# Optimization experiments

Hardware: AMD Instinct MI355X
Metric: run time of the kernel (lower is better)

Reference implementation:

```python
import jax, jax.numpy as jnp
import numpy as np

B, C, H, W = 8, 512, 32, 32
HEADS, GROUPS = 8, 32
EPS = 1e-5


def setup_inputs() -> dict:
    key = jax.random.key(0)
    ks = jax.random.split(key, 6)
    s = 0.02
    return {
        "x": jax.random.normal(ks[0], (B, C, H, W), jnp.float32),
        "gn_scale": jnp.ones((C,), jnp.float32),
        "gn_bias": jnp.zeros((C,), jnp.float32),
        "wq": jax.random.normal(ks[1], (C, C), jnp.float32) * s,
        "bq": jnp.zeros((C,), jnp.float32),
        "wk": jax.random.normal(ks[2], (C, C), jnp.float32) * s,
        "bk": jnp.zeros((C,), jnp.float32),
        "wv": jax.random.normal(ks[3], (C, C), jnp.float32) * s,
        "bv": jnp.zeros((C,), jnp.float32),
        "wo": jax.random.normal(ks[4], (C, C), jnp.float32) * s,
        "bo": jnp.zeros((C,), jnp.float32),
    }


def reference(x, gn_scale, gn_bias, wq, bq, wk, bk, wv, bv, wo, bo):
    b, c, h, w = x.shape
    n = h * w
    cdh = c // HEADS
    xf = x.reshape(b, c, n)

    # GroupNorm over (channels_per_group, spatial)
    g = xf.reshape(b, GROUPS, (c // GROUPS) * n)
    mu = g.mean(-1, keepdims=True)
    var = g.var(-1, keepdims=True)
    hn = ((g - mu) * jax.lax.rsqrt(var + EPS)).reshape(b, c, n)
    hn = hn * gn_scale[:, None] + gn_bias[:, None]

    # 1x1 conv projections == channel-mixing GEMMs
    q = jnp.einsum('oc,bcn->bon', wq, hn) + bq[:, None]
    k = jnp.einsum('oc,bcn->bon', wk, hn) + bk[:, None]
    v = jnp.einsum('oc,bcn->bon', wv, hn) + bv[:, None]

    qh = q.reshape(b, HEADS, cdh, n)
    kh = k.reshape(b, HEADS, cdh, n)
    vh = v.reshape(b, HEADS, cdh, n)

    scale = 1.0 / jnp.sqrt(jnp.float32(cdh))
    scores = jnp.einsum('bhdq,bhdk->bhqk', qh, kh) * scale  # [B,H,N,N]
    attn = jax.nn.softmax(scores, axis=-1)  # dropout p=0.0 (eval) -> identity

    oh = jnp.einsum('bhqk,bhdk->bhdq', attn, vh).reshape(b, c, n)
    out = jnp.einsum('oc,bcn->bon', wo, oh) + bo[:, None]
    return (xf + out).reshape(b, c, h, w)
```

## Files before the change

### kernel.cpp

```cpp
#include <hip/hip_runtime.h>

#define BB 8
#define CC 512
#define NSP 1024
#define HEADS 8
#define DH 64
#define NGROUPS 32
#define CPG 16
#define GN_EPS 1e-5f
#define MQKV 1536

typedef __attribute__((ext_vector_type(8))) short bf16x8;
typedef __attribute__((ext_vector_type(4))) short short4v;
typedef __attribute__((ext_vector_type(4))) float f32x4;

typedef __attribute__((address_space(3))) unsigned int lds_u32;
typedef const __attribute__((address_space(1))) unsigned int glb_u32;

__device__ __forceinline__ short f2bf(float f) {
    union { float f; unsigned u; } v; v.f = f;
    unsigned r = v.u + 0x7fffu + ((v.u >> 16) & 1u);
    return (short)(r >> 16);
}
__device__ __forceinline__ short f2bf_trunc(float f) {
    union { float f; unsigned u; } v; v.f = f;
    return (short)(v.u >> 16);
}

__device__ __forceinline__ float wave_reduce_sum(float v) {
    #pragma unroll
    for (int off = 32; off > 0; off >>= 1) v += __shfl_down(v, off, 64);
    return v;
}

#define QSCALE 0.18033688011112042f

__global__ __launch_bounds__(256) void convert_w_kernel(
        const float* __restrict__ wq, const float* __restrict__ wk,
        const float* __restrict__ wv, const float* __restrict__ wo,
        const float* __restrict__ bq, const float* __restrict__ bk,
        const float* __restrict__ bv,
        short* __restrict__ wqkv, short* __restrict__ wob,
        float* __restrict__ bqkv) {
    const int gid = blockIdx.x * 256 + threadIdx.x;
    if (gid < MQKV * CC) {
        const int r = gid >> 9;
        const int cc = gid & 511;
        const float* src = (r < 512) ? wq : ((r < 1024) ? wk : wv);
        float v = src[(size_t)(r & 511) * CC + cc];
        if (r < 512) v *= QSCALE;
        wqkv[gid] = f2bf(v);
    } else {
        const int g2 = gid - MQKV * CC;
        wob[g2] = f2bf(wo[g2]);
    }
    if (gid < MQKV) {
        float bvv = (gid < 512) ? bq[gid] * QSCALE
                  : ((gid < 1024) ? bk[gid - 512] : bv[gid - 1024]);
        bqkv[gid] = bvv;
    }
}

__global__ __launch_bounds__(256) void groupnorm_t_kernel(
        const float* __restrict__ x, const float* __restrict__ gsc,
        const float* __restrict__ gbi, short* __restrict__ hnt) {
    const int b = blockIdx.x >> 5, g = blockIdx.x & 31;
    const int count = CPG * NSP;
    const size_t base = ((size_t)b * CC + (size_t)g * CPG) * NSP;
    float s = 0.f, ss = 0.f;
    for (int i = threadIdx.x; i < count; i += 256) {
        float v = x[base + i];
        s += v; ss += v * v;
    }
    __shared__ float red[2][4];
    s = wave_reduce_sum(s); ss = wave_reduce_sum(ss);
    const int wid = threadIdx.x >> 6, lane = threadIdx.x & 63;
    if (lane == 0) { red[0][wid] = s; red[1][wid] = ss; }
    __syncthreads();
    if (threadIdx.x == 0) {
        float ts  = red[0][0] + red[0][1] + red[0][2] + red[0][3];
        float tss = red[1][0] + red[1][1] + red[1][2] + red[1][3];
        float mu = ts / count;
        float var = tss / count - mu * mu;
        red[0][0] = mu;
        red[1][0] = rsqrtf(var + GN_EPS);
    }
    __syncthreads();
    const float mu = red[0][0], rstd = red[1][0];
    float sc[16], bi[16];
    #pragma unroll
    for (int ci = 0; ci < 16; ++ci) {
        sc[ci] = gsc[g * CPG + ci] * rstd;
        bi[ci] = gbi[g * CPG + ci];
    }
    for (int n0 = 0; n0 < NSP; n0 += 256) {
        const int n = n0 + threadIdx.x;
        short tmp[16];
        #pragma unroll
        for (int ci = 0; ci < 16; ++ci) {
            float v = x[base + (size_t)ci * NSP + n];
            tmp[ci] = f2bf((v - mu) * sc[ci] + bi[ci]);
        }
        const size_t ob = ((size_t)b * NSP + n) * CC + g * CPG;
        *(bf16x8*)&hnt[ob]     = *(bf16x8*)&tmp[0];
        *(bf16x8*)&hnt[ob + 8] = *(bf16x8*)&tmp[8];
    }
}

template <int MODE>
__global__ __launch_bounds__(256) void gemm_bt_kernel(
        const short* __restrict__ A, const float* __restrict__ bias,
        const short* __restrict__ Bt, void* __restrict__ Yv,
        const float* __restrict__ res, short* __restrict__ qt,
        short* __restrict__ kt, int M) {
    __shared__ short As[128 * 64];
    __shared__ short Bs[128 * 64];
    const int nt = blockIdx.x;
    const int b = nt >> 3, n0 = (nt & 7) * 128;
    const int o0 = blockIdx.y * 128;
    const int t = threadIdx.x, w = t >> 6, lane = t & 63;
    const int quad = lane >> 4, l16 = lane & 15;
    const int wm = w & 1, wn = w >> 1;
    const int srow = lane >> 3, scol = (lane & 7) * 8;

    f32x4 acc[4][4];
    #pragma unroll
    for (int i = 0; i < 4; ++i)
        #pragma unroll
        for (int j = 0; j < 4; ++j) acc[i][j] = (f32x4){0.f, 0.f, 0.f, 0.f};

    const short* Ab = A + (size_t)o0 * 512;
    const short* Bb = Bt + ((size_t)b * 1024 + n0) * 512;

    for (int k0 = 0; k0 < 512; k0 += 64) {
        #pragma unroll
        for (int i = 0; i < 4; ++i) {
            const int r0 = w * 32 + i * 8;
            __builtin_amdgcn_global_load_lds(
                (glb_u32*)(Ab + (size_t)(r0 + srow) * 512 + k0 + scol),
                (lds_u32*)&As[r0 * 64], 16, 0, 0);
            __builtin_amdgcn_global_load_lds(
                (glb_u32*)(Bb + (size_t)(r0 + srow) * 512 + k0 + scol),
                (lds_u32*)&Bs[r0 * 64], 16, 0, 0);
        }
        __syncthreads();

        bf16x8 af[4][2], bfr[4][2];
        #pragma unroll
        for (int mi = 0; mi < 4; ++mi)
            #pragma unroll
            for (int s = 0; s < 2; ++s)
                af[mi][s] = *(bf16x8*)&As[(wm * 64 + mi * 16 + l16) * 64 + quad * 8 + s * 32];
        #pragma unroll
        for (int ni = 0; ni < 4; ++ni)
            #pragma unroll
            for (int s = 0; s < 2; ++s)
                bfr[ni][s] = *(bf16x8*)&Bs[(wn * 64 + ni * 16 + l16) * 64 + quad * 8 + s * 32];
        #pragma unroll
        for (int mi = 0; mi < 4; ++mi)
            #pragma unroll
            for (int ni = 0; ni < 4; ++ni)
                #pragma unroll
                for (int s = 0; s < 2; ++s)
                    acc[mi][ni] = __builtin_amdgcn_mfma_f32_16x16x32_bf16(
                        af[mi][s], bfr[ni][s], acc[mi][ni], 0, 0, 0);
        __syncthreads();
    }

    if (MODE == 0 && o0 < 1024) {
        short* T = (o0 < 512) ? qt : kt;
        const int hh = ((o0 & 511) + wm * 64) >> 6;
        const size_t hb = ((size_t)b * HEADS + hh) * NSP;
        #pragma unroll
        for (int mi = 0; mi < 4; ++mi) {
            const int dh0 = mi * 16 + quad * 4;
            #pragma unroll
            for (int ni = 0; ni < 4; ++ni) {
                const int n = n0 + wn * 64 + ni * 16 + l16;
                short pk[4];
                #pragma unroll
                for (int r = 0; r < 4; ++r)
                    pk[r] = f2bf(acc[mi][ni][r] + bias[o0 + wm * 64 + dh0 + r]);
                *(short4v*)&kt[0];
                *(short4v*)&T[(hb + n) * DH + dh0] = *(short4v*)pk;
            }
        }
        return;
    }

    #pragma unroll
    for (int mi = 0; mi < 4; ++mi) {
        #pragma unroll
        for (int r = 0; r < 4; ++r) {
            const int m = wm * 64 + mi * 16 + quad * 4 + r;
            const float bv = bias[o0 + m];
            const size_t rowb = ((size_t)b * M + o0 + m) * 1024 + n0;
            if (MODE == 0) {
                short* Y = (short*)Yv;
                #pragma unroll
                for (int ni = 0; ni < 4; ++ni) {
                    const int n = wn * 64 + ni * 16 + l16;
                    Y[rowb + n] = f2bf(acc[mi][ni][r] + bv);
                }
            } else {
                float* Y = (float*)Yv;
                #pragma unroll
                for (int ni = 0; ni < 4; ++ni) {
                    const int n = wn * 64 + ni * 16 + l16;
                    Y[rowb + n] = acc[mi][ni][r] + bv + res[rowb + n];
                }
            }
        }
    }
}

__global__ __launch_bounds__(256) void attn_mfma_kernel(
        const short* __restrict__ qkv, const short* __restrict__ qt,
        const short* __restrict__ kt, short* __restrict__ obt) {
    __shared__ short Ks[64][68];
    __shared__ short Vs[64][68];
    __shared__ short Ps[4][16][68];
    const int id = blockIdx.x;
    const int xcd = id & 7, j = id >> 3;
    const int q0 = (j & 15) * 64;
    const int hi = (j >> 4) * 8 + xcd;
    const int b = hi >> 3, h = hi & 7;
    const int t = threadIdx.x;
    const int w = t >> 6, lane = t & 63;
    const int quad = lane >> 4, l16 = lane & 15;
    const size_t vbase = ((size_t)b * MQKV + 1024 + h * DH) * NSP;
    const size_t hb = ((size_t)b * HEADS + h) * NSP;
    const int qrow = q0 + w * 16 + l16;

    bf16x8 qf[2];
    #pragma unroll
    for (int s = 0; s < 2; ++s)
        qf[s] = *(const bf16x8*)&qt[(hb + qrow) * DH + quad * 8 + 32 * s];

    float lsum = 0.f;
    f32x4 oacc[4];
    #pragma unroll
    for (int i = 0; i < 4; ++i) oacc[i] = (f32x4){0.f, 0.f, 0.f, 0.f};

    for (int k0 = 0; k0 < NSP; k0 += 64) {
        __syncthreads();
        #pragma unroll
        for (int p = 0; p < 2; ++p) {
            int idx = t + p * 256;
            int row = idx >> 3, c8 = (idx & 7) * 8;
            *(bf16x8*)&Ks[row][c8] =
                *(const bf16x8*)&kt[(hb + k0 + row) * DH + c8];
        }
        #pragma unroll
        for (int p = 0; p < 2; ++p) {
            int idx = t + p * 256;
            int d = idx >> 3, k8 = (idx & 7) * 8;
            *(bf16x8*)&Vs[d][k8] =
                *(const bf16x8*)(qkv + vbase + (size_t)d * NSP + k0 + k8);
        }
        __syncthreads();

        f32x4 st[4];
        #pragma unroll
        for (int ks = 0; ks < 4; ++ks) {
            f32x4 a2 = (f32x4){0.f, 0.f, 0.f, 0.f};
            a2 = __builtin_amdgcn_mfma_f32_16x16x32_bf16(
                *(bf16x8*)&Ks[ks * 16 + l16][quad * 8], qf[0], a2, 0, 0, 0);
            a2 = __builtin_amdgcn_mfma_f32_16x16x32_bf16(
                *(bf16x8*)&Ks[ks * 16 + l16][quad * 8 + 32], qf[1], a2, 0, 0, 0);
            st[ks] = a2;
        }

        short pb[16];
        #pragma unroll
        for (int ks = 0; ks < 4; ++ks)
            #pragma unroll
            for (int r = 0; r < 4; ++r) {
                float p = exp2f(st[ks][r]);
                lsum += p;
                pb[ks * 4 + r] = f2bf_trunc(p);
            }
        #pragma unroll
        for (int ks = 0; ks < 4; ++ks)
            *(short4v*)&Ps[w][l16][ks * 16 + quad * 4] = *(short4v*)&pb[ks * 4];
        bf16x8 pf0 = *(bf16x8*)&Ps[w][l16][quad * 8];
        bf16x8 pf1 = *(bf16x8*)&Ps[w][l16][quad * 8 + 32];

        #pragma unroll
        for (int ds = 0; ds < 4; ++ds) {
            oacc[ds] = __builtin_amdgcn_mfma_f32_16x16x32_bf16(
                *(bf16x8*)&Vs[ds * 16 + l16][quad * 8], pf0, oacc[ds], 0, 0, 0);
            oacc[ds] = __builtin_amdgcn_mfma_f32_16x16x32_bf16(
                *(bf16x8*)&Vs[ds * 16 + l16][quad * 8 + 32], pf1, oacc[ds], 0, 0, 0);
        }
    }

    lsum += __shfl_xor(lsum, 16, 64);
    lsum += __shfl_xor(lsum, 32, 64);
    const float inv = 1.0f / lsum;
    #pragma unroll
    for (int ds = 0; ds < 4; ++ds) {
        short o4[4];
        #pragma unroll
        for (int r = 0; r < 4; ++r) o4[r] = f2bf(oacc[ds][r] * inv);
        *(short4v*)&obt[((size_t)b * NSP + qrow) * CC + h * DH + ds * 16 + quad * 4] =
            *(short4v*)o4;
    }
}

extern "C" void kernel_launch(void* const* d_in, const int* in_sizes, int n_in,
                              void* d_out, int out_size, void* d_ws, size_t ws_size,
                              hipStream_t stream) {
    const float* x   = (const float*)d_in[0];
    const float* gsc = (const float*)d_in[1];
    const float* gbi = (const float*)d_in[2];
    const float* wq  = (const float*)d_in[3];
    const float* bq  = (const float*)d_in[4];
    const float* wk  = (const float*)d_in[5];
    const float* bk  = (const float*)d_in[6];
    const float* wv  = (const float*)d_in[7];
    const float* bv  = (const float*)d_in[8];
    const float* wo  = (const float*)d_in[9];
    const float* bo  = (const float*)d_in[10];
    float* out = (float*)d_out;

    short* wqkv_bf = (short*)d_ws;
    short* wo_bf   = wqkv_bf + (size_t)MQKV * CC;
    float* bqkv    = (float*)(wo_bf + (size_t)CC * CC);
    short* hnt     = (short*)(bqkv + MQKV);
    short* qkv     = hnt + (size_t)BB * NSP * CC;
    short* obt     = qkv + (size_t)BB * MQKV * NSP;
    short* kt      = obt + (size_t)BB * NSP * CC;
    short* qt      = kt + (size_t)BB * HEADS * NSP * DH;

    convert_w_kernel<<<(MQKV * CC + CC * CC) / 256, 256, 0, stream>>>(
        wq, wk, wv, wo, bq, bk, bv, wqkv_bf, wo_bf, bqkv);

    groupnorm_t_kernel<<<BB * NGROUPS, 256, 0, stream>>>(x, gsc, gbi, hnt);

    dim3 qkvgrid(64, MQKV / 128);
    gemm_bt_kernel<0><<<qkvgrid, 256, 0, stream>>>(
        wqkv_bf, bqkv, hnt, (void*)qkv, nullptr, qt, kt, MQKV);

    attn_mfma_kernel<<<1024, 256, 0, stream>>>(qkv, qt, kt, obt);

    dim3 wogrid(64, CC / 128);
    gemm_bt_kernel<1><<<wogrid, 256, 0, stream>>>(
        wo_bf, bo, obt, (void*)out, x, nullptr, nullptr, CC);
}
```

Baseline: 199.6 us.

## Double query rows per attention wave, async swizzled K/V loads, LDS-staged Q/K stores

Each wave in the attention kernel now handles 32 query rows instead of 16, so every K/V fragment read from LDS feeds twice as many MFMAs, and the grid is halved to 512 blocks. K and V tiles are loaded straight into LDS with global_load_lds, using an XOR swizzle in place of padding to avoid bank conflicts. The QKV GEMM epilogue stages Q/K tiles through shared memory so they can be written with coalesced 16-byte stores instead of scattered 8-byte ones. The cost is higher register pressure, fewer blocks to fill the GPU, and extra barriers in the GEMM epilogue.

```diff
diff --git a/kernel.cpp b/kernel.cpp
--- a/kernel.cpp
+++ b/kernel.cpp
@@ -113,8 +113,9 @@
         const short* __restrict__ Bt, void* __restrict__ Yv,
         const float* __restrict__ res, short* __restrict__ qt,
         short* __restrict__ kt, int M) {
-    __shared__ short As[128 * 64];
-    __shared__ short Bs[128 * 64];
+    __shared__ short SM[2 * 128 * 64];
+    short* As = SM;
+    short* Bs = SM + 128 * 64;
     const int nt = blockIdx.x;
     const int b = nt >> 3, n0 = (nt & 7) * 128;
     const int o0 = blockIdx.y * 128;
@@ -169,20 +170,35 @@
 
     if (MODE == 0 && o0 < 1024) {
         short* T = (o0 < 512) ? qt : kt;
-        const int hh = ((o0 & 511) + wm * 64) >> 6;
-        const size_t hb = ((size_t)b * HEADS + hh) * NSP;
-        #pragma unroll
-        for (int mi = 0; mi < 4; ++mi) {
-            const int dh0 = mi * 16 + quad * 4;
-            #pragma unroll
-            for (int ni = 0; ni < 4; ++ni) {
-                const int n = n0 + wn * 64 + ni * 16 + l16;
-                short pk[4];
-                #pragma unroll
-                for (int r = 0; r < 4; ++r)
-                    pk[r] = f2bf(acc[mi][ni][r] + bias[o0 + wm * 64 + dh0 + r]);
-                *(short4v*)&kt[0];
-                *(short4v*)&T[(hb + n) * DH + dh0] = *(short4v*)pk;
+        #pragma unroll
+        for (int pass = 0; pass < 2; ++pass) {
+            __syncthreads();
+            if (wm == pass) {
+                #pragma unroll
+                for (int mi = 0; mi < 4; ++mi) {
+                    const int d0 = mi * 16 + quad * 4;
+                    float bv[4];
+                    #pragma unroll
+                    for (int r = 0; r < 4; ++r) bv[r] = bias[o0 + pass * 64 + d0 + r];
+                    #pragma unroll
+                    for (int ni = 0; ni < 4; ++ni) {
+                        const int nl = wn * 64 + ni * 16 + l16;
+                        short pk[4];
+                        #pragma unroll
+                        for (int r = 0; r < 4; ++r)
+                            pk[r] = f2bf(acc[mi][ni][r] + bv[r]);
+                        *(short4v*)&SM[nl * 68 + d0] = *(short4v*)pk;
+                    }
+                }
+            }
+            __syncthreads();
+            const int hh = ((o0 & 511) >> 6) + pass;
+            const size_t hb2 = ((size_t)b * HEADS + hh) * NSP;
+            #pragma unroll
+            for (int it = 0; it < 4; ++it) {
+                const int rr = (t >> 3) + it * 32;
+                const int cc = (t & 7) * 8;
+                *(bf16x8*)&T[(hb2 + n0 + rr) * DH + cc] = *(bf16x8*)&SM[rr * 68 + cc];
             }
         }
         return;
@@ -217,94 +233,115 @@
 __global__ __launch_bounds__(256) void attn_mfma_kernel(
         const short* __restrict__ qkv, const short* __restrict__ qt,
         const short* __restrict__ kt, short* __restrict__ obt) {
-    __shared__ short Ks[64][68];
-    __shared__ short Vs[64][68];
-    __shared__ short Ps[4][16][68];
+    __shared__ short Ks[64 * 64];
+    __shared__ short Vs[64 * 64];
+    __shared__ short Ps[4][32][68];
     const int id = blockIdx.x;
     const int xcd = id & 7, j = id >> 3;
-    const int q0 = (j & 15) * 64;
-    const int hi = (j >> 4) * 8 + xcd;
+    const int q0 = (j & 7) * 128;
+    const int hi = (j >> 3) * 8 + xcd;
     const int b = hi >> 3, h = hi & 7;
     const int t = threadIdx.x;
     const int w = t >> 6, lane = t & 63;
     const int quad = lane >> 4, l16 = lane & 15;
     const size_t vbase = ((size_t)b * MQKV + 1024 + h * DH) * NSP;
     const size_t hb = ((size_t)b * HEADS + h) * NSP;
-    const int qrow = q0 + w * 16 + l16;
-
-    bf16x8 qf[2];
-    #pragma unroll
-    for (int s = 0; s < 2; ++s)
-        qf[s] = *(const bf16x8*)&qt[(hb + qrow) * DH + quad * 8 + 32 * s];
-
-    float lsum = 0.f;
-    f32x4 oacc[4];
-    #pragma unroll
-    for (int i = 0; i < 4; ++i) oacc[i] = (f32x4){0.f, 0.f, 0.f, 0.f};
+    const int sc = (lane & 7) ^ (lane >> 3);
+    const int swz0 = (quad ^ (l16 & 7)) * 8;
+    const int swz1 = ((quad + 4) ^ (l16 & 7)) * 8;
+
+    bf16x8 qf[2][2];
+    #pragma unroll
+    for (int g = 0; g < 2; ++g)
+        #pragma unroll
+        for (int s = 0; s < 2; ++s)
+            qf[g][s] = *(const bf16x8*)&qt[(hb + q0 + w * 32 + g * 16 + l16) * DH
+                                           + quad * 8 + 32 * s];
+
+    float lsum[2] = {0.f, 0.f};
+    f32x4 oacc[2][4];
+    #pragma unroll
+    for (int g = 0; g < 2; ++g)
+        #pragma unroll
+        for (int i = 0; i < 4; ++i) oacc[g][i] = (f32x4){0.f, 0.f, 0.f, 0.f};
 
     for (int k0 = 0; k0 < NSP; k0 += 64) {
         __syncthreads();
         #pragma unroll
         for (int p = 0; p < 2; ++p) {
-            int idx = t + p * 256;
-            int row = idx >> 3, c8 = (idx & 7) * 8;
-            *(bf16x8*)&Ks[row][c8] =
-                *(const bf16x8*)&kt[(hb + k0 + row) * DH + c8];
-        }
-        #pragma unroll
-        for (int p = 0; p < 2; ++p) {
-            int idx = t + p * 256;
-            int d = idx >> 3, k8 = (idx & 7) * 8;
-            *(bf16x8*)&Vs[d][k8] =
-                *(const bf16x8*)(qkv + vbase + (size_t)d * NSP + k0 + k8);
+            const int row = w * 16 + p * 8 + (lane >> 3);
+            __builtin_amdgcn_global_load_lds(
+                (glb_u32*)(kt + (hb + k0 + row) * DH + sc * 8),
+                (lds_u32*)(Ks + w * 1024 + p * 512), 16, 0, 0);
+            __builtin_amdgcn_global_load_lds(
+                (glb_u32*)(qkv + vbase + (size_t)row * NSP + k0 + sc * 8),
+                (lds_u32*)(Vs + w * 1024 + p * 512), 16, 0, 0);
         }
         __syncthreads();
 
-        f32x4 st[4];
+        f32x4 st[2][4];
         #pragma unroll
         for (int ks = 0; ks < 4; ++ks) {
-            f32x4 a2 = (f32x4){0.f, 0.f, 0.f, 0.f};
-            a2 = __builtin_amdgcn_mfma_f32_16x16x32_bf16(
-                *(bf16x8*)&Ks[ks * 16 + l16][quad * 8], qf[0], a2, 0, 0, 0);
-            a2 = __builtin_amdgcn_mfma_f32_16x16x32_bf16(
-                *(bf16x8*)&Ks[ks * 16 + l16][quad * 8 + 32], qf[1], a2, 0, 0, 0);
-            st[ks] = a2;
-        }
-
-        short pb[16];
-        #pragma unroll
-        for (int ks = 0; ks < 4; ++ks)
-            #pragma unroll
-            for (int r = 0; r < 4; ++r) {
-                float p = exp2f(st[ks][r]);
-                lsum += p;
-                pb[ks * 4 + r] = f2bf_trunc(p);
-            }
-        #pragma unroll
-        for (int ks = 0; ks < 4; ++ks)
-            *(short4v*)&Ps[w][l16][ks * 16 + quad * 4] = *(short4v*)&pb[ks * 4];
-        bf16x8 pf0 = *(bf16x8*)&Ps[w][l16][quad * 8];
-        bf16x8 pf1 = *(bf16x8*)&Ps[w][l16][quad * 8 + 32];
+            bf16x8 ka0 = *(bf16x8*)&Ks[(ks * 16 + l16) * 64 + swz0];
+            bf16x8 ka1 = *(bf16x8*)&Ks[(ks * 16 + l16) * 64 + swz1];
+            #pragma unroll
+            for (int g = 0; g < 2; ++g) {
+                f32x4 a2 = (f32x4){0.f, 0.f, 0.f, 0.f};
+                a2 = __builtin_amdgcn_mfma_f32_16x16x32_bf16(ka0, qf[g][0], a2, 0, 0, 0);
+                a2 = __builtin_amdgcn_mfma_f32_16x16x32_bf16(ka1, qf[g][1], a2, 0, 0, 0);
+                st[g][ks] = a2;
+            }
+        }
+
+        #pragma unroll
+        for (int g = 0; g < 2; ++g) {
+            short pb[16];
+            #pragma unroll
+            for (int ks = 0; ks < 4; ++ks)
+                #pragma unroll
+                for (int r = 0; r < 4; ++r) {
+                    float p = exp2f(st[g][ks][r]);
+                    lsum[g] += p;
+                    pb[ks * 4 + r] = f2bf_trunc(p);
+                }
+            #pragma unroll
+            for (int ks = 0; ks < 4; ++ks)
+                *(short4v*)&Ps[w][g * 16 + l16][ks * 16 + quad * 4] = *(short4v*)&pb[ks * 4];
+        }
+        bf16x8 pf[2][2];
+        #pragma unroll
+        for (int g = 0; g < 2; ++g)
+            #pragma unroll
+            for (int s = 0; s < 2; ++s)
+                pf[g][s] = *(bf16x8*)&Ps[w][g * 16 + l16][quad * 8 + 32 * s];
 
         #pragma unroll
         for (int ds = 0; ds < 4; ++ds) {
-            oacc[ds] = __builtin_amdgcn_mfma_f32_16x16x32_bf16(
-                *(bf16x8*)&Vs[ds * 16 + l16][quad * 8], pf0, oacc[ds], 0, 0, 0);
-            oacc[ds] = __builtin_amdgcn_mfma_f32_16x16x32_bf16(
-                *(bf16x8*)&Vs[ds * 16 + l16][quad * 8 + 32], pf1, oacc[ds], 0, 0, 0);
-        }
-    }
-
-    lsum += __shfl_xor(lsum, 16, 64);
-    lsum += __shfl_xor(lsum, 32, 64);
-    const float inv = 1.0f / lsum;
-    #pragma unroll
-    for (int ds = 0; ds < 4; ++ds) {
-        short o4[4];
-        #pragma unroll
-        for (int r = 0; r < 4; ++r) o4[r] = f2bf(oacc[ds][r] * inv);
-        *(short4v*)&obt[((size_t)b * NSP + qrow) * CC + h * DH + ds * 16 + quad * 4] =
-            *(short4v*)o4;
+            bf16x8 va0 = *(bf16x8*)&Vs[(ds * 16 + l16) * 64 + swz0];
+            bf16x8 va1 = *(bf16x8*)&Vs[(ds * 16 + l16) * 64 + swz1];
+            #pragma unroll
+            for (int g = 0; g < 2; ++g) {
+                oacc[g][ds] = __builtin_amdgcn_mfma_f32_16x16x32_bf16(va0, pf[g][0], oacc[g][ds], 0, 0, 0);
+                oacc[g][ds] = __builtin_amdgcn_mfma_f32_16x16x32_bf16(va1, pf[g][1], oacc[g][ds], 0, 0, 0);
+            }
+        }
+    }
+
+    #pragma unroll
+    for (int g = 0; g < 2; ++g) {
+        float ls = lsum[g];
+        ls += __shfl_xor(ls, 16, 64);
+        ls += __shfl_xor(ls, 32, 64);
+        const float inv = 1.0f / ls;
+        const int qrow = q0 + w * 32 + g * 16 + l16;
+        #pragma unroll
+        for (int ds = 0; ds < 4; ++ds) {
+            short o4[4];
+            #pragma unroll
+            for (int r = 0; r < 4; ++r) o4[r] = f2bf(oacc[g][ds][r] * inv);
+            *(short4v*)&obt[((size_t)b * NSP + qrow) * CC + h * DH + ds * 16 + quad * 4] =
+                *(short4v*)o4;
+        }
     }
 }
 
@@ -342,7 +379,7 @@
     gemm_bt_kernel<0><<<qkvgrid, 256, 0, stream>>>(
         wqkv_bf, bqkv, hnt, (void*)qkv, nullptr, qt, kt, MQKV);
 
-    attn_mfma_kernel<<<1024, 256, 0, stream>>>(qkv, qt, kt, obt);
+    attn_mfma_kernel<<<512, 256, 0, stream>>>(qkv, qt, kt, obt);
 
     dim3 wogrid(64, CC / 128);
     gemm_bt_kernel<1><<<wogrid, 256, 0, stream>>>(
```

Result: faster. 193.2 us (-3.2%).
